# Optimization experiments

Hardware: AMD Instinct MI355X
Metric: run time of the kernel (lower is better)

## Reference

```python
import jax, jax.numpy as jnp
import numpy as np

N_NODES = 50000
N_EDGES = 800000
DIM = 128
HEADS = 4
NEG_SLOPE = 0.2
LN_EPS = 1e-5


def setup_inputs() -> dict:
    key = jax.random.key(0)
    ks = jax.random.split(key, 8)
    x = jax.random.normal(ks[0], (N_NODES, DIM), dtype=jnp.float32)
    edge_index = jax.random.randint(ks[1], (2, N_EDGES), 0, N_NODES, dtype=jnp.int32)
    W = jax.random.normal(ks[2], (DIM, DIM), dtype=jnp.float32) * (1.0 / np.sqrt(DIM))
    b = jnp.zeros((DIM,), dtype=jnp.float32)
    C = DIM // HEADS
    att_src = jax.random.normal(ks[3], (HEADS, C), dtype=jnp.float32) * 0.1
    att_dst = jax.random.normal(ks[4], (HEADS, C), dtype=jnp.float32) * 0.1
    ln_gamma = jnp.ones((DIM,), dtype=jnp.float32)
    ln_beta = jnp.zeros((DIM,), dtype=jnp.float32)
    prelu_w = jnp.full((1,), 0.25, dtype=jnp.float32)
    return {"x": x, "edge_index": edge_index, "W": W, "b": b,
            "att_src": att_src, "att_dst": att_dst,
            "ln_gamma": ln_gamma, "ln_beta": ln_beta, "prelu_w": prelu_w}


def reference(x, edge_index, W, b, att_src, att_dst, ln_gamma, ln_beta, prelu_w):
    N, D = x.shape
    H = HEADS
    C = D // H
    # shared linear transform (PyG GATConv lin_src == lin_dst for homogeneous input)
    xw = (x @ W).reshape(N, H, C)                      # [N,H,C]
    a_src = jnp.einsum('nhc,hc->nh', xw, att_src)      # [N,H]
    a_dst = jnp.einsum('nhc,hc->nh', xw, att_dst)      # [N,H]
    # add self loops (PyG default add_self_loops=True)
    loop = jnp.arange(N, dtype=edge_index.dtype)
    src = jnp.concatenate([edge_index[0], loop])       # [E+N]
    dst = jnp.concatenate([edge_index[1], loop])       # [E+N]
    # per-edge attention logits + segment softmax over destination
    alpha = jax.nn.leaky_relu(a_src[src] + a_dst[dst], NEG_SLOPE)   # [E+N,H]
    amax = jax.ops.segment_max(alpha, dst, num_segments=N)          # [N,H]
    alpha = jnp.exp(alpha - amax[dst])
    denom = jax.ops.segment_sum(alpha, dst, num_segments=N)         # [N,H]
    alpha = alpha / denom[dst]
    # weighted aggregation of source features
    msg = xw[src] * alpha[:, :, None]                               # [E+N,H,C]
    out = jax.ops.segment_sum(msg, dst, num_segments=N).reshape(N, D) + b
    # residual + LayerNorm + PReLU
    h = x + out
    mu = jnp.mean(h, axis=-1, keepdims=True)
    var = jnp.mean(jnp.square(h - mu), axis=-1, keepdims=True)
    h = (h - mu) * jax.lax.rsqrt(var + LN_EPS) * ln_gamma + ln_beta
    return jnp.where(h > 0, h, prelu_w[0] * h)
```

## Files before the change

### kernel.cpp

```cpp
#include <hip/hip_runtime.h>

#define NNODES 50000
#define NEDGES 800000
#define NEDGE4 200000
#define DIMF 128
#define NHEADS 4
#define NEG_SLOPE 0.2f
#define LN_EPS 1e-5f
#define SLOTS 64
#define NPERX 6250
#define CSRBLK 2048

typedef int   v4i   __attribute__((ext_vector_type(4)));
typedef float v2f   __attribute__((ext_vector_type(2)));
typedef short bf16x8 __attribute__((ext_vector_type(8)));
typedef float f32x4  __attribute__((ext_vector_type(4)));

__device__ __forceinline__ unsigned short f2bf(float f) {
    unsigned int u = __float_as_uint(f);
    u = (u + 0x7fffu + ((u >> 16) & 1u)) >> 16;
    return (unsigned short)u;
}

__global__ __launch_bounds__(256) void k_linear(
    const float* __restrict__ x, const float* __restrict__ W,
    const float* __restrict__ att_src, const float* __restrict__ att_dst,
    unsigned short* __restrict__ xwb,
    float* __restrict__ asrc, float* __restrict__ adst,
    int* __restrict__ cursor)
{
    __shared__ unsigned short Wt[128][136];
    const int tid  = threadIdx.x;
    const int base = blockIdx.x * 64;

    if (tid < 64 && base + tid < NNODES) cursor[base + tid] = 0;

    {
        const float4* W4 = (const float4*)W;
        const int nq = tid & 31;
        int k = tid >> 5;
        #pragma unroll
        for (int it = 0; it < 16; ++it, k += 8) {
            float4 wv = W4[k * 32 + nq];
            Wt[nq * 4 + 0][k] = f2bf(wv.x);
            Wt[nq * 4 + 1][k] = f2bf(wv.y);
            Wt[nq * 4 + 2][k] = f2bf(wv.z);
            Wt[nq * 4 + 3][k] = f2bf(wv.w);
        }
    }
    __syncthreads();

    const int wv_   = tid >> 6;
    const int lane  = tid & 63;
    const int row16 = lane & 15;
    const int kg    = lane >> 4;
    const int grow_a = base + wv_ * 16 + row16;
    const int arow   = (grow_a < NNODES) ? grow_a : 0;

    f32x4 acc[8];
    #pragma unroll
    for (int ct = 0; ct < 8; ++ct) acc[ct] = (f32x4){0.f, 0.f, 0.f, 0.f};

    #pragma unroll
    for (int ks = 0; ks < 4; ++ks) {
        const float4* xr = (const float4*)(x + (size_t)arow * DIMF + ks * 32 + kg * 8);
        const float4 xa = xr[0], xb = xr[1];
        bf16x8 af;
        af[0] = (short)f2bf(xa.x); af[1] = (short)f2bf(xa.y);
        af[2] = (short)f2bf(xa.z); af[3] = (short)f2bf(xa.w);
        af[4] = (short)f2bf(xb.x); af[5] = (short)f2bf(xb.y);
        af[6] = (short)f2bf(xb.z); af[7] = (short)f2bf(xb.w);
        #pragma unroll
        for (int ct = 0; ct < 8; ++ct) {
            const bf16x8 bfr = *(const bf16x8*)&Wt[ct * 16 + row16][ks * 32 + kg * 8];
            acc[ct] = __builtin_amdgcn_mfma_f32_16x16x32_bf16(af, bfr, acc[ct], 0, 0, 0);
        }
    }

    #pragma unroll
    for (int ct = 0; ct < 8; ++ct) {
        const int col = ct * 16 + row16;
        #pragma unroll
        for (int r = 0; r < 4; ++r) {
            const int grow = base + wv_ * 16 + kg * 4 + r;
            if (grow < NNODES)
                xwb[(size_t)grow * DIMF + col] = f2bf(acc[ct][r]);
        }
    }

    float ps[4][4], pd[4][4];
    #pragma unroll
    for (int h = 0; h < 4; ++h)
        #pragma unroll
        for (int r = 0; r < 4; ++r) { ps[h][r] = 0.f; pd[h][r] = 0.f; }
    #pragma unroll
    for (int ct = 0; ct < 8; ++ct) {
        const int h    = ct >> 1;
        const int cmod = (ct & 1) * 16 + row16;
        const float aS = att_src[h * 32 + cmod];
        const float aD = att_dst[h * 32 + cmod];
        #pragma unroll
        for (int r = 0; r < 4; ++r) {
            ps[h][r] += acc[ct][r] * aS;
            pd[h][r] += acc[ct][r] * aD;
        }
    }
    #pragma unroll
    for (int o = 1; o < 16; o <<= 1) {
        #pragma unroll
        for (int h = 0; h < 4; ++h)
            #pragma unroll
            for (int r = 0; r < 4; ++r) {
                ps[h][r] += __shfl_xor(ps[h][r], o);
                pd[h][r] += __shfl_xor(pd[h][r], o);
            }
    }
    if (row16 == 0) {
        #pragma unroll
        for (int r = 0; r < 4; ++r) {
            const int grow = base + wv_ * 16 + kg * 4 + r;
            if (grow < NNODES) {
                ((float4*)asrc)[grow] = make_float4(ps[0][r], ps[1][r], ps[2][r], ps[3][r]);
                ((float4*)adst)[grow] = make_float4(pd[0][r], pd[1][r], pd[2][r], pd[3][r]);
            }
        }
    }
}

__global__ __launch_bounds__(256) void k_scatter(
    const int* __restrict__ esrc, const int* __restrict__ edst,
    int* __restrict__ cursor, unsigned short* __restrict__ perm)
{
    const int lo = (blockIdx.x & 7) * NPERX, hi = lo + NPERX;
    const int stride = (CSRBLK >> 3) * 256;
    const v4i* es4 = (const v4i*)esrc;
    const v4i* ed4 = (const v4i*)edst;
    for (int e = (blockIdx.x >> 3) * 256 + threadIdx.x; e < NEDGE4; e += stride) {
        v4i d4 = __builtin_nontemporal_load(ed4 + e);
        v4i s4 = __builtin_nontemporal_load(es4 + e);
        #pragma unroll
        for (int c = 0; c < 4; ++c) {
            const int dd = d4[c], ss = s4[c];
            if (dd >= lo && dd < hi) {
                int p = atomicAdd(&cursor[dd], 1);
                if (p < SLOTS) perm[(size_t)dd * SLOTS + p] = (unsigned short)ss;
            }
        }
    }
}

__global__ __launch_bounds__(256) void k_weights(
    const float4* __restrict__ asrc4, const float4* __restrict__ adst4,
    const int* __restrict__ cursor, const unsigned short* __restrict__ perm,
    ushort4* __restrict__ wperm)
{
    const int wid  = (blockIdx.x * 256 + threadIdx.x) >> 6;
    const int lane = threadIdx.x & 63;
    if (wid >= NNODES) return;

    int cnt = cursor[wid];
    if (cnt > SLOTS) cnt = SLOTS;
    const float4 dv = adst4[wid];

    ushort4 wu = make_ushort4(0, 0, 0, 0);
    if (lane < cnt) {
        const int s = (int)perm[(size_t)wid * SLOTS + lane];
        const float4 ae = asrc4[s];
        float l0 = ae.x + dv.x, l1 = ae.y + dv.y;
        float l2 = ae.z + dv.z, l3 = ae.w + dv.w;
        l0 = (l0 > 0.f) ? l0 : NEG_SLOPE * l0;
        l1 = (l1 > 0.f) ? l1 : NEG_SLOPE * l1;
        l2 = (l2 > 0.f) ? l2 : NEG_SLOPE * l2;
        l3 = (l3 > 0.f) ? l3 : NEG_SLOPE * l3;
        wu.x = f2bf(__expf(l0)); wu.y = f2bf(__expf(l1));
        wu.z = f2bf(__expf(l2)); wu.w = f2bf(__expf(l3));
    }
    wperm[(size_t)wid * SLOTS + lane] = wu;
}

__global__ __launch_bounds__(256) void k_gat(
    const float* __restrict__ x, const float* __restrict__ bias,
    const float* __restrict__ asrc, const float* __restrict__ adst,
    const unsigned int* __restrict__ xwb,
    const int* __restrict__ cursor, const unsigned short* __restrict__ perm,
    const unsigned short* __restrict__ wperm_u16,
    const float* __restrict__ ln_g, const float* __restrict__ ln_b,
    const float* __restrict__ prelu_w, float* __restrict__ out)
{
    const int wid  = (blockIdx.x * 256 + threadIdx.x) >> 6;
    const int lane = threadIdx.x & 63;
    if (wid >= NNODES) return;
    const int myh = lane >> 4;
    const int hb  = lane & 3;

    const float adh_b = adst[wid * NHEADS + hb];
    float lgS = asrc[wid * NHEADS + hb] + adh_b;
    lgS = (lgS > 0.f) ? lgS : NEG_SLOPE * lgS;
    const float wself_b = __expf(lgS);

    int cnt = cursor[wid];
    if (cnt > SLOTS) cnt = SLOTS;
    const int sidx = (lane < cnt) ? (int)perm[(size_t)wid * SLOTS + lane] : 0;

    const float wself = __shfl(wself_b, myh);
    const unsigned int vself = xwb[(size_t)wid * 64 + lane];
    float acc0 = wself * __uint_as_float(vself << 16);
    float acc1 = wself * __uint_as_float(vself & 0xffff0000u);
    float dsum = 0.f;

    const int jmax = (cnt + 15) >> 4;
    for (int j = 0; j < jmax; ++j) {
        const unsigned short wu = wperm_u16[(size_t)wid * 256 + j * 64 + lane];
        const float wv = __uint_as_float(((unsigned)wu) << 16);
        dsum += wv;

        #pragma unroll
        for (int b = 0; b < 2; ++b) {
            const int ebase = j * 16 + b * 8;
            int s_[8]; float w_[8]; unsigned v_[8];
            #pragma unroll
            for (int e = 0; e < 8; ++e) {
                s_[e] = __shfl(sidx, ebase + e);
                w_[e] = __shfl(wv, ((b * 8 + e) << 2) | myh);
            }
            #pragma unroll
            for (int e = 0; e < 8; ++e)
                v_[e] = xwb[(size_t)s_[e] * 64 + lane];
            #pragma unroll
            for (int e = 0; e < 8; ++e) {
                acc0 += w_[e] * __uint_as_float(v_[e] << 16);
                acc1 += w_[e] * __uint_as_float(v_[e] & 0xffff0000u);
            }
        }
    }

    #pragma unroll
    for (int o = 4; o < 64; o <<= 1) dsum += __shfl_xor(dsum, o);
    const float wsum = __shfl(dsum + wself_b, myh);

    const float inv = 1.0f / wsum;
    const int c = lane * 2;
    const float2 xr = ((const float2*)x)[(size_t)wid * 64 + lane];
    float h0 = xr.x + acc0 * inv + bias[c];
    float h1 = xr.y + acc1 * inv + bias[c + 1];

    float s1 = h0 + h1, s2 = h0 * h0 + h1 * h1;
    #pragma unroll
    for (int o = 1; o < 64; o <<= 1) {
        s1 += __shfl_xor(s1, o);
        s2 += __shfl_xor(s2, o);
    }
    const float mu  = s1 * (1.f / 128.f);
    const float var = s2 * (1.f / 128.f) - mu * mu;
    const float r   = rsqrtf(var + LN_EPS);

    float g0 = (h0 - mu) * r * ln_g[c]     + ln_b[c];
    float g1 = (h1 - mu) * r * ln_g[c + 1] + ln_b[c + 1];
    const float pw = prelu_w[0];
    g0 = (g0 > 0.f) ? g0 : pw * g0;
    g1 = (g1 > 0.f) ? g1 : pw * g1;

    v2f gv; gv.x = g0; gv.y = g1;
    __builtin_nontemporal_store(gv, (v2f*)out + (size_t)wid * 64 + lane);
}

extern "C" void kernel_launch(void* const* d_in, const int* in_sizes, int n_in,
                              void* d_out, int out_size, void* d_ws, size_t ws_size,
                              hipStream_t stream)
{
    const float* x    = (const float*)d_in[0];
    const int*   eidx = (const int*)  d_in[1];
    const float* W    = (const float*)d_in[2];
    const float* bias = (const float*)d_in[3];
    const float* attS = (const float*)d_in[4];
    const float* attD = (const float*)d_in[5];
    const float* lng  = (const float*)d_in[6];
    const float* lnb  = (const float*)d_in[7];
    const float* pre  = (const float*)d_in[8];

    const int* esrc = eidx;
    const int* edst = eidx + NEDGES;

    unsigned short* xwb = (unsigned short*)d_ws;
    float* asrc    = (float*)(xwb + (size_t)NNODES * DIMF);
    float* adst    = asrc + (size_t)NNODES * NHEADS;
    int*   cursor  = (int*)(adst + (size_t)NNODES * NHEADS);
    unsigned short* perm = (unsigned short*)(cursor + NNODES);
    ushort4* wperm = (ushort4*)(perm + (size_t)NNODES * SLOTS);

    k_linear<<<dim3((NNODES + 63) / 64), dim3(256), 0, stream>>>(
        x, W, attS, attD, xwb, asrc, adst, cursor);

    k_scatter<<<dim3(CSRBLK), dim3(256), 0, stream>>>(esrc, edst, cursor, perm);

    k_weights<<<dim3((NNODES * 64 + 255) / 256), dim3(256), 0, stream>>>(
        (const float4*)asrc, (const float4*)adst, cursor, perm, wperm);

    k_gat<<<dim3((NNODES * 64 + 255) / 256), dim3(256), 0, stream>>>(
        x, bias, asrc, adst, (const unsigned int*)xwb, cursor, perm,
        (const unsigned short*)wperm, lng, lnb, pre, (float*)d_out);
}
```

Baseline: 123.0 us.

## Replace filtered multi-pass edge scatter with two-phase bucket binning

New measurement: 160.3 us. 30.3% more time.

```diff
diff --git a/kernel.cpp b/kernel.cpp
--- a/kernel.cpp
+++ b/kernel.cpp
@@ -2,14 +2,15 @@
 
 #define NNODES 50000
 #define NEDGES 800000
-#define NEDGE4 200000
 #define DIMF 128
 #define NHEADS 4
 #define NEG_SLOPE 0.2f
 #define LN_EPS 1e-5f
 #define SLOTS 64
-#define NPERX 6250
-#define CSRBLK 2048
+#define NBUCK 7
+#define BCAP  140000
+#define BINBLK 512
+#define SC2BLK 1024
 
 typedef int   v4i   __attribute__((ext_vector_type(4)));
 typedef float v2f   __attribute__((ext_vector_type(2)));
@@ -27,13 +28,14 @@
     const float* __restrict__ att_src, const float* __restrict__ att_dst,
     unsigned short* __restrict__ xwb,
     float* __restrict__ asrc, float* __restrict__ adst,
-    int* __restrict__ cursor)
+    int* __restrict__ cursor, int* __restrict__ btail)
 {
     __shared__ unsigned short Wt[128][136];
     const int tid  = threadIdx.x;
     const int base = blockIdx.x * 64;
 
     if (tid < 64 && base + tid < NNODES) cursor[base + tid] = 0;
+    if (blockIdx.x == 0 && tid >= 64 && tid < 72) btail[tid - 64] = 0;
 
     {
         const float4* W4 = (const float4*)W;
@@ -127,25 +129,60 @@
     }
 }
 
-__global__ __launch_bounds__(256) void k_scatter(
+__global__ __launch_bounds__(256) void k_bin(
     const int* __restrict__ esrc, const int* __restrict__ edst,
+    unsigned int* __restrict__ bins, int* __restrict__ btail)
+{
+    __shared__ unsigned int lb[NBUCK][256];
+    __shared__ int lcnt[NBUCK];
+    __shared__ int lbase[NBUCK];
+    const int tid = threadIdx.x;
+
+    if (tid < NBUCK) lcnt[tid] = 0;
+    __syncthreads();
+
+    for (int base = blockIdx.x * 256; base < NEDGES; base += BINBLK * 256) {
+        const int e = base + tid;
+        if (e < NEDGES) {
+            const int dd = edst[e], ss = esrc[e];
+            const int b = dd >> 13;
+            const unsigned int pk = ((unsigned int)dd << 16) | (unsigned int)ss;
+            const int pos = atomicAdd(&lcnt[b], 1);
+            lb[b][pos] = pk;
+        }
+        __syncthreads();
+        if (tid < NBUCK) {
+            const int c = lcnt[tid];
+            lbase[tid] = (c > 0) ? atomicAdd(&btail[tid], c) : 0;
+        }
+        __syncthreads();
+        #pragma unroll
+        for (int b2 = 0; b2 < NBUCK; ++b2) {
+            const int c = lcnt[b2], bs = lbase[b2];
+            for (int i = tid; i < c; i += 256)
+                if (bs + i < BCAP)
+                    bins[(size_t)b2 * BCAP + bs + i] = lb[b2][i];
+        }
+        __syncthreads();
+        if (tid < NBUCK) lcnt[tid] = 0;
+        __syncthreads();
+    }
+}
+
+__global__ __launch_bounds__(256) void k_scatter2(
+    const unsigned int* __restrict__ bins, const int* __restrict__ btail,
     int* __restrict__ cursor, unsigned short* __restrict__ perm)
 {
-    const int lo = (blockIdx.x & 7) * NPERX, hi = lo + NPERX;
-    const int stride = (CSRBLK >> 3) * 256;
-    const v4i* es4 = (const v4i*)esrc;
-    const v4i* ed4 = (const v4i*)edst;
-    for (int e = (blockIdx.x >> 3) * 256 + threadIdx.x; e < NEDGE4; e += stride) {
-        v4i d4 = __builtin_nontemporal_load(ed4 + e);
-        v4i s4 = __builtin_nontemporal_load(es4 + e);
-        #pragma unroll
-        for (int c = 0; c < 4; ++c) {
-            const int dd = d4[c], ss = s4[c];
-            if (dd >= lo && dd < hi) {
-                int p = atomicAdd(&cursor[dd], 1);
-                if (p < SLOTS) perm[(size_t)dd * SLOTS + p] = (unsigned short)ss;
-            }
-        }
+    const int b = blockIdx.x & 7;
+    if (b >= NBUCK) return;
+    const int n = btail[b] < BCAP ? btail[b] : BCAP;
+    const unsigned int* bb = bins + (size_t)b * BCAP;
+    const int stride = (SC2BLK >> 3) * 256;
+    for (int i = (blockIdx.x >> 3) * 256 + threadIdx.x; i < n; i += stride) {
+        const unsigned int pk = __builtin_nontemporal_load(bb + i);
+        const int dd = pk >> 16, ss = pk & 0xffffu;
+        const int p = atomicAdd(&cursor[dd], 1);
+        if (p < SLOTS) perm[(size_t)dd * SLOTS + p] = (unsigned short)ss;
     }
 }
 
@@ -286,12 +323,16 @@
     float* adst    = asrc + (size_t)NNODES * NHEADS;
     int*   cursor  = (int*)(adst + (size_t)NNODES * NHEADS);
     unsigned short* perm = (unsigned short*)(cursor + NNODES);
-    ushort4* wperm = (ushort4*)(perm + (size_t)NNODES * SLOTS);
+    int*   btail   = (int*)(perm + (size_t)NNODES * SLOTS);
+    ushort4* wperm = (ushort4*)(btail + 16);
+    unsigned int* bins = (unsigned int*)wperm;
 
     k_linear<<<dim3((NNODES + 63) / 64), dim3(256), 0, stream>>>(
-        x, W, attS, attD, xwb, asrc, adst, cursor);
-
-    k_scatter<<<dim3(CSRBLK), dim3(256), 0, stream>>>(esrc, edst, cursor, perm);
+        x, W, attS, attD, xwb, asrc, adst, cursor, btail);
+
+    k_bin<<<dim3(BINBLK), dim3(256), 0, stream>>>(esrc, edst, bins, btail);
+
+    k_scatter2<<<dim3(SC2BLK), dim3(256), 0, stream>>>(bins, btail, cursor, perm);
 
     k_weights<<<dim3((NNODES * 64 + 255) / 256), dim3(256), 0, stream>>>(
         (const float4*)asrc, (const float4*)adst, cursor, perm, wperm);
```

## Fuse linear projection and edge scatter into one concurrent launch

Applied to the files above, without the earlier changes.

After: 113.9 us. 1.08x faster.

```diff
diff --git a/kernel.cpp b/kernel.cpp
--- a/kernel.cpp
+++ b/kernel.cpp
@@ -9,44 +9,75 @@
 #define LN_EPS 1e-5f
 #define SLOTS 64
 #define NPERX 6250
-#define CSRBLK 2048
+#define NLB 782
+#define SCB 2048
 
 typedef int   v4i   __attribute__((ext_vector_type(4)));
 typedef float v2f   __attribute__((ext_vector_type(2)));
 typedef short bf16x8 __attribute__((ext_vector_type(8)));
 typedef float f32x4  __attribute__((ext_vector_type(4)));
+typedef unsigned short u16x8 __attribute__((ext_vector_type(8)));
 
 __device__ __forceinline__ unsigned short f2bf(float f) {
     unsigned int u = __float_as_uint(f);
     u = (u + 0x7fffu + ((u >> 16) & 1u)) >> 16;
     return (unsigned short)u;
 }
-
-__global__ __launch_bounds__(256) void k_linear(
-    const float* __restrict__ x, const float* __restrict__ W,
+__device__ __forceinline__ float bf2f(unsigned short u) {
+    return __uint_as_float(((unsigned int)u) << 16);
+}
+
+__global__ __launch_bounds__(256) void k_prep(const float* __restrict__ W,
+                                              unsigned short* __restrict__ WtG)
+{
+    const int idx = blockIdx.x * 256 + threadIdx.x;
+    if (idx < DIMF * DIMF) {
+        const int k = idx >> 7, col = idx & 127;
+        WtG[col * 136 + k] = f2bf(W[idx]);
+    }
+}
+
+__global__ __launch_bounds__(256) void k_main(
+    const float* __restrict__ x, const unsigned short* __restrict__ WtG,
     const float* __restrict__ att_src, const float* __restrict__ att_dst,
     unsigned short* __restrict__ xwb,
     float* __restrict__ asrc, float* __restrict__ adst,
-    int* __restrict__ cursor)
-{
-    __shared__ unsigned short Wt[128][136];
-    const int tid  = threadIdx.x;
+    const int* __restrict__ esrc, const int* __restrict__ edst,
+    int* __restrict__ cursor, unsigned short* __restrict__ perm)
+{
+    __shared__ unsigned short WtL[128 * 136];
+    __shared__ float sAttS[128], sAttD[128];
+    const int tid = threadIdx.x;
+
+    if (blockIdx.x >= NLB) {
+        const int vb = blockIdx.x - NLB;
+        const int lo = (blockIdx.x & 7) * NPERX, hi = lo + NPERX;
+        const v4i* es4 = (const v4i*)esrc;
+        const v4i* ed4 = (const v4i*)edst;
+        const int stride = (SCB >> 3) * 256;
+        for (int e = (vb >> 3) * 256 + tid; e < NEDGE4; e += stride) {
+            v4i d4 = __builtin_nontemporal_load(ed4 + e);
+            v4i s4 = __builtin_nontemporal_load(es4 + e);
+            #pragma unroll
+            for (int c = 0; c < 4; ++c) {
+                const int dd = d4[c], ss = s4[c];
+                if (dd >= lo && dd < hi) {
+                    int p = atomicAdd(&cursor[dd], 1);
+                    if (p < SLOTS) perm[(size_t)dd * SLOTS + p] = (unsigned short)ss;
+                }
+            }
+        }
+        return;
+    }
+
     const int base = blockIdx.x * 64;
 
-    if (tid < 64 && base + tid < NNODES) cursor[base + tid] = 0;
-
+    if (tid < 128) sAttS[tid] = att_src[tid];
+    else           sAttD[tid - 128] = att_dst[tid - 128];
     {
-        const float4* W4 = (const float4*)W;
-        const int nq = tid & 31;
-        int k = tid >> 5;
-        #pragma unroll
-        for (int it = 0; it < 16; ++it, k += 8) {
-            float4 wv = W4[k * 32 + nq];
-            Wt[nq * 4 + 0][k] = f2bf(wv.x);
-            Wt[nq * 4 + 1][k] = f2bf(wv.y);
-            Wt[nq * 4 + 2][k] = f2bf(wv.z);
-            Wt[nq * 4 + 3][k] = f2bf(wv.w);
-        }
+        const uint4* g = (const uint4*)WtG;
+        uint4* l = (uint4*)WtL;
+        for (int i = tid; i < 2176; i += 256) l[i] = g[i];
     }
     __syncthreads();
 
@@ -72,80 +103,41 @@
         af[6] = (short)f2bf(xb.z); af[7] = (short)f2bf(xb.w);
         #pragma unroll
         for (int ct = 0; ct < 8; ++ct) {
-            const bf16x8 bfr = *(const bf16x8*)&Wt[ct * 16 + row16][ks * 32 + kg * 8];
+            const bf16x8 bfr = *(const bf16x8*)&WtL[(ct * 16 + row16) * 136 + ks * 32 + kg * 8];
             acc[ct] = __builtin_amdgcn_mfma_f32_16x16x32_bf16(af, bfr, acc[ct], 0, 0, 0);
         }
     }
 
+    __syncthreads();
+    unsigned short* OutL = WtL;
     #pragma unroll
     for (int ct = 0; ct < 8; ++ct) {
-        const int col = ct * 16 + row16;
-        #pragma unroll
-        for (int r = 0; r < 4; ++r) {
-            const int grow = base + wv_ * 16 + kg * 4 + r;
-            if (grow < NNODES)
-                xwb[(size_t)grow * DIMF + col] = f2bf(acc[ct][r]);
-        }
-    }
-
-    float ps[4][4], pd[4][4];
-    #pragma unroll
-    for (int h = 0; h < 4; ++h)
-        #pragma unroll
-        for (int r = 0; r < 4; ++r) { ps[h][r] = 0.f; pd[h][r] = 0.f; }
-    #pragma unroll
-    for (int ct = 0; ct < 8; ++ct) {
-        const int h    = ct >> 1;
-        const int cmod = (ct & 1) * 16 + row16;
-        const float aS = att_src[h * 32 + cmod];
-        const float aD = att_dst[h * 32 + cmod];
-        #pragma unroll
-        for (int r = 0; r < 4; ++r) {
-            ps[h][r] += acc[ct][r] * aS;
-            pd[h][r] += acc[ct][r] * aD;
-        }
-    }
-    #pragma unroll
-    for (int o = 1; o < 16; o <<= 1) {
-        #pragma unroll
-        for (int h = 0; h < 4; ++h)
-            #pragma unroll
-            for (int r = 0; r < 4; ++r) {
-                ps[h][r] += __shfl_xor(ps[h][r], o);
-                pd[h][r] += __shfl_xor(pd[h][r], o);
-            }
-    }
-    if (row16 == 0) {
-        #pragma unroll
-        for (int r = 0; r < 4; ++r) {
-            const int grow = base + wv_ * 16 + kg * 4 + r;
-            if (grow < NNODES) {
-                ((float4*)asrc)[grow] = make_float4(ps[0][r], ps[1][r], ps[2][r], ps[3][r]);
-                ((float4*)adst)[grow] = make_float4(pd[0][r], pd[1][r], pd[2][r], pd[3][r]);
-            }
-        }
-    }
-}
-
-__global__ __launch_bounds__(256) void k_scatter(
-    const int* __restrict__ esrc, const int* __restrict__ edst,
-    int* __restrict__ cursor, unsigned short* __restrict__ perm)
-{
-    const int lo = (blockIdx.x & 7) * NPERX, hi = lo + NPERX;
-    const int stride = (CSRBLK >> 3) * 256;
-    const v4i* es4 = (const v4i*)esrc;
-    const v4i* ed4 = (const v4i*)edst;
-    for (int e = (blockIdx.x >> 3) * 256 + threadIdx.x; e < NEDGE4; e += stride) {
-        v4i d4 = __builtin_nontemporal_load(ed4 + e);
-        v4i s4 = __builtin_nontemporal_load(es4 + e);
-        #pragma unroll
-        for (int c = 0; c < 4; ++c) {
-            const int dd = d4[c], ss = s4[c];
-            if (dd >= lo && dd < hi) {
-                int p = atomicAdd(&cursor[dd], 1);
-                if (p < SLOTS) perm[(size_t)dd * SLOTS + p] = (unsigned short)ss;
-            }
-        }
+        #pragma unroll
+        for (int r = 0; r < 4; ++r)
+            OutL[(wv_ * 16 + kg * 4 + r) * 136 + ct * 16 + row16] = f2bf(acc[ct][r]);
+    }
+    __syncthreads();
+
+    const int row = tid >> 2, seg = tid & 3;
+    const int grow = base + row;
+    if (grow < NNODES) {
+        const u16x8* srcv = (const u16x8*)&OutL[row * 136 + seg * 32];
+        u16x8* dstv = (u16x8*)(xwb + (size_t)grow * DIMF + seg * 32);
+        float ps = 0.f, pd = 0.f;
+        #pragma unroll
+        for (int q = 0; q < 4; ++q) {
+            const u16x8 v = srcv[q];
+            dstv[q] = v;
+            #pragma unroll
+            for (int j = 0; j < 8; ++j) {
+                const float f = bf2f(v[j]);
+                const int c = seg * 32 + q * 8 + j;
+                ps += f * sAttS[c];
+                pd += f * sAttD[c];
+            }
+        }
+        asrc[grow * NHEADS + seg] = ps;
+        adst[grow * NHEADS + seg] = pd;
     }
 }
 
@@ -287,11 +279,14 @@
     int*   cursor  = (int*)(adst + (size_t)NNODES * NHEADS);
     unsigned short* perm = (unsigned short*)(cursor + NNODES);
     ushort4* wperm = (ushort4*)(perm + (size_t)NNODES * SLOTS);
-
-    k_linear<<<dim3((NNODES + 63) / 64), dim3(256), 0, stream>>>(
-        x, W, attS, attD, xwb, asrc, adst, cursor);
-
-    k_scatter<<<dim3(CSRBLK), dim3(256), 0, stream>>>(esrc, edst, cursor, perm);
+    unsigned short* WtG = (unsigned short*)(wperm + (size_t)NNODES * SLOTS);
+
+    hipMemsetAsync(cursor, 0, (size_t)NNODES * sizeof(int), stream);
+
+    k_prep<<<dim3(64), dim3(256), 0, stream>>>(W, WtG);
+
+    k_main<<<dim3(NLB + SCB), dim3(256), 0, stream>>>(
+        x, WtG, attS, attD, xwb, asrc, adst, esrc, edst, cursor, perm);
 
     k_weights<<<dim3((NNODES * 64 + 255) / 256), dim3(256), 0, stream>>>(
         (const float4*)asrc, (const float4*)adst, cursor, perm, wperm);
```
